# Kernel tuning notes

Measured on AMD Instinct MI355X. Metric: run time of the kernel, lower is better.

The kernel has to match this reference:

```python
import jax, jax.numpy as jnp
import numpy as np


def setup_inputs() -> dict:
    key = jax.random.key(0)
    ks = jax.random.split(key, 7)
    O, I, K = 64, 64, 3
    D = K * K
    x = jax.random.normal(ks[0], (32, I, 224, 224), jnp.float32)
    weight_loc = jax.random.normal(ks[1], (O, I, K, K), jnp.float32) * 0.05
    weight_L = jax.random.normal(ks[2], (O, I, D, D), jnp.float32) * 0.05
    bias_loc = jax.random.normal(ks[3], (O,), jnp.float32) * 0.05
    bias_ro = jax.random.normal(ks[4], (O,), jnp.float32) * 0.05
    eps_w = jax.random.normal(ks[5], (O, I, D), jnp.float32)
    eps_b = jax.random.normal(ks[6], (O,), jnp.float32)
    return {"x": x, "weight_loc": weight_loc, "weight_L": weight_L,
            "bias_loc": bias_loc, "bias_ro": bias_ro,
            "eps_w": eps_w, "eps_b": eps_b}


def reference(x, weight_loc, weight_L, bias_loc, bias_ro, eps_w, eps_b):
    # weight_loc: [O, I, K, K]; weight_L: [O, I, D, D] with D = K*K
    O, I, K, _ = weight_loc.shape
    D = K * K
    # diag_softplus: softplus on the diagonal of each per-(o,i) scale_tril,
    # keep strictly-lower part; MVN uses the lower-triangular scale_tril.
    diag = jnp.diagonal(weight_L, axis1=-2, axis2=-1)            # [O, I, D]
    eye = jnp.eye(D, dtype=weight_L.dtype)
    L = jnp.tril(weight_L, -1) + jax.nn.softplus(diag)[..., None] * eye  # [O, I, D, D]
    # Batched MVN rsample: loc + L @ eps, collapsing the O*I Python loop
    w = weight_loc + jnp.einsum('oiab,oib->oia', L, eps_w).reshape(O, I, K, K)
    # Bias rsample: loc + eps * softplus(ro)
    b = bias_loc + eps_b * jax.nn.softplus(bias_ro)              # [O]
    out = jax.lax.conv_general_dilated(
        x, w, window_strides=(1, 1), padding='SAME',
        dimension_numbers=('NCHW', 'OIHW', 'NCHW'))
    return out + b[None, :, None, None]
```

## Files before the change

### kernel.cpp

```cpp
#include <hip/hip_runtime.h>
#include <hip/hip_bf16.h>
#include <stdint.h>

typedef short bhalf8 __attribute__((ext_vector_type(8)));
typedef float facc4 __attribute__((ext_vector_type(4)));
typedef unsigned int uintv2 __attribute__((ext_vector_type(2)));

static __device__ __forceinline__ unsigned short f2bfu(float f) {
  return __builtin_bit_cast(unsigned short, __float2bfloat16(f));
}

__global__ void prep_kernel(const float* __restrict__ wloc,
                            const float* __restrict__ wL,
                            const float* __restrict__ eps_w,
                            const float* __restrict__ bloc,
                            const float* __restrict__ bro,
                            const float* __restrict__ eps_b,
                            short* __restrict__ wt, float* __restrict__ bias) {
  int t = blockIdx.x * 256 + threadIdx.x;
  int o = t >> 6, i = t & 63;
  int kc = i >> 5, il = i & 31;
  const float* Lp = wL + (size_t)t * 81;
  const float* ep = eps_w + (size_t)t * 9;
  const float* lp = wloc + (size_t)t * 9;
  float e[9];
#pragma unroll
  for (int b = 0; b < 9; ++b) e[b] = ep[b];
#pragma unroll
  for (int a = 0; a < 9; ++a) {
    float s = lp[a];
    for (int b = 0; b < a; ++b) s += Lp[a * 9 + b] * e[b];
    float d = Lp[a * 9 + a];
    float sp = (d > 20.f) ? d : log1pf(expf(d));
    s += sp * e[a];
    wt[((a * 2 + kc) * 64 + o) * 32 + il] = (short)f2bfu(s);
  }
  if (t < 64) {
    float d = bro[t];
    float sp = (d > 20.f) ? d : log1pf(expf(d));
    bias[t] = bloc[t] + eps_b[t] * sp;
  }
}

#define XBUF 10880

#define LD1(cj, i)                                                    \
  ((hok && (w_in0 + (i)) >= 0 && (w_in0 + (i)) < 224)                 \
       ? cbase[(size_t)(cj)*50176 + w_in0 + (i)]                      \
       : 0.f)

__global__ __launch_bounds__(512, 4) void conv_fused_kernel(
    const float* __restrict__ x, const short* __restrict__ wtg,
    const float* __restrict__ bias, float* __restrict__ out) {
  extern __shared__ short smem[];
  short* lds_x = smem;
  short* lds_w = smem + 21760;

  int b0 = blockIdx.x;
  int b = (b0 & 7) * 784 + (b0 >> 3);
  int ht = b % 28;
  int rest = b / 28;
  int wc = rest % 7, n = rest / 7;
  int h0 = ht * 8, w0 = wc * 32;
  int t = threadIdx.x, lane = t & 63, wv = t >> 6;
  int l15 = lane & 15, l4 = lane >> 4;

#define LOADX(V, ic_)                                                       \
  do {                                                                      \
    _Pragma("unroll") for (int k = 0; k < 2; ++k) {                         \
      int u = t + k * 512;                                                  \
      if (u < 720) {                                                        \
        int chg = u & 7, tmp = u >> 3;                                      \
        int ccg = tmp % 9, r = tmp / 9;                                     \
        int h_in = h0 - 1 + r;                                              \
        bool hok = (h_in >= 0) & (h_in < 224);                              \
        int w_in0 = w0 - 1 + ccg * 4;                                       \
        const float* cbase =                                                \
            x + ((size_t)(n * 64 + (ic_)*32 + chg * 4) * 224 +              \
                 (hok ? h_in : 0)) *                                        \
                    224;                                                    \
        if (hok && w_in0 >= 0 && w_in0 + 3 < 224) {                         \
          V[k][0] = *(const float4*)(cbase + w_in0);                        \
          V[k][1] = *(const float4*)(cbase + 50176 + w_in0);                \
          V[k][2] = *(const float4*)(cbase + 2 * 50176 + w_in0);            \
          V[k][3] = *(const float4*)(cbase + 3 * 50176 + w_in0);            \
        } else {                                                            \
          V[k][0] = make_float4(LD1(0, 0), LD1(0, 1), LD1(0, 2), LD1(0, 3)); \
          V[k][1] = make_float4(LD1(1, 0), LD1(1, 1), LD1(1, 2), LD1(1, 3)); \
          V[k][2] = make_float4(LD1(2, 0), LD1(2, 1), LD1(2, 2), LD1(2, 3)); \
          V[k][3] = make_float4(LD1(3, 0), LD1(3, 1), LD1(3, 2), LD1(3, 3)); \
        }                                                                   \
      }                                                                     \
    }                                                                       \
  } while (0)

#define CVTW(bufsel, V)                                                     \
  do {                                                                      \
    short* lx_ = lds_x + (bufsel)*XBUF;                                     \
    _Pragma("unroll") for (int k = 0; k < 2; ++k) {                         \
      int u = t + k * 512;                                                  \
      if (u < 720) {                                                        \
        int chg = u & 7, tmp = u >> 3;                                      \
        int ccg = tmp % 9, r = tmp / 9;                                     \
        int g = chg >> 1, hs = (chg & 1) << 2;                              \
        _Pragma("unroll") for (int i = 0; i < 4; ++i) {                     \
          int cc = ccg * 4 + i;                                             \
          if (cc < 34) {                                                    \
            float a0 = ((const float*)&V[k][0])[i];                         \
            float a1 = ((const float*)&V[k][1])[i];                         \
            float a2 = ((const float*)&V[k][2])[i];                         \
            float a3 = ((const float*)&V[k][3])[i];                         \
            unsigned int p0 =                                               \
                (unsigned int)f2bfu(a0) | ((unsigned int)f2bfu(a1) << 16);  \
            unsigned int p1 =                                               \
                (unsigned int)f2bfu(a2) | ((unsigned int)f2bfu(a3) << 16);  \
            uintv2 pk = {p0, p1};                                           \
            *(uintv2*)(lx_ + (((r * 4 + g) * 34 + cc) << 3) + hs) = pk;     \
          }                                                                 \
        }                                                                   \
      }                                                                     \
    }                                                                       \
  } while (0)

#define STAGE_W(ic_)                                                        \
  do {                                                                      \
    _Pragma("unroll") for (int k = 0; k < 5; ++k) {                         \
      int id = k * 512 + t;                                                 \
      if (id < 2304) {                                                      \
        int a_ = id >> 8, rem_ = id & 255;                                  \
        int g_ = rem_ >> 6, o_ = rem_ & 63;                                 \
        const short* src =                                                  \
            wtg + ((a_ * 2 + (ic_)) * 64 + o_) * 32 + g_ * 8;               \
        __builtin_amdgcn_global_load_lds(                                   \
            (const __attribute__((address_space(1))) void*)src,             \
            (__attribute__((address_space(3))) void*)(lds_w +               \
                                                      (k * 512 + wv * 64) * \
                                                          8),               \
            16, 0, 0);                                                      \
      }                                                                     \
    }                                                                       \
  } while (0)

  facc4 acc[4][2];
#pragma unroll
  for (int om = 0; om < 4; ++om)
#pragma unroll
    for (int p = 0; p < 2; ++p) {
      facc4 z = {0.f, 0.f, 0.f, 0.f};
      acc[om][p] = z;
    }

#define COMPUTE(bufsel)                                                     \
  do {                                                                      \
    const short* bx = lds_x + (bufsel)*XBUF;                                \
    __builtin_amdgcn_s_setprio(1);                                          \
    _Pragma("unroll") for (int kh = 0; kh < 3; ++kh) {                      \
      int r = wv + kh;                                                      \
      _Pragma("unroll") for (int kw = 0; kw < 3; ++kw) {                    \
        const int a_ = kh * 3 + kw;                                         \
        bhalf8 av[4];                                                       \
        _Pragma("unroll") for (int om = 0; om < 4; ++om) av[om] =           \
            *(const bhalf8*)(lds_w +                                        \
                             ((a_ * 4 + l4) * 64 + om * 16 + l15) * 8);     \
        _Pragma("unroll") for (int p = 0; p < 2; ++p) {                     \
          int tc = p * 16 + l15 + kw;                                       \
          bhalf8 bv = *(const bhalf8*)(bx + ((r * 4 + l4) * 34 + tc) * 8);  \
          _Pragma("unroll") for (int om = 0; om < 4; ++om) acc[om][p] =     \
              __builtin_amdgcn_mfma_f32_16x16x32_bf16(av[om], bv,           \
                                                      acc[om][p], 0, 0, 0); \
        }                                                                   \
      }                                                                     \
    }                                                                       \
    __builtin_amdgcn_s_setprio(0);                                          \
  } while (0)

  float4 xv[2][4];

  STAGE_W(0);
  LOADX(xv, 0);
  CVTW(0, xv);
  asm volatile("s_waitcnt vmcnt(0)" ::: "memory");
  __syncthreads();

  LOADX(xv, 1);
  __builtin_amdgcn_sched_barrier(0);
  COMPUTE(0);
  __builtin_amdgcn_s_barrier();
  __builtin_amdgcn_sched_barrier(0);
  STAGE_W(1);
  CVTW(1, xv);
  asm volatile("s_waitcnt vmcnt(0)" ::: "memory");
  __syncthreads();
  COMPUTE(1);

#undef LOADX
#undef CVTW
#undef STAGE_W
#undef COMPUTE

  int h = h0 + wv;
#pragma unroll
  for (int om = 0; om < 4; ++om) {
#pragma unroll
    for (int jj = 0; jj < 4; ++jj) {
      int o = om * 16 + l4 * 4 + jj;
      float bo = bias[o];
      float* op = out + ((size_t)(n * 64 + o) * 224 + h) * 224 + w0;
#pragma unroll
      for (int p = 0; p < 2; ++p) op[p * 16 + l15] = acc[om][p][jj] + bo;
    }
  }
}

extern "C" void kernel_launch(void* const* d_in, const int* in_sizes, int n_in,
                              void* d_out, int out_size, void* d_ws,
                              size_t ws_size, hipStream_t stream) {
  const float* x = (const float*)d_in[0];
  const float* wloc = (const float*)d_in[1];
  const float* wL = (const float*)d_in[2];
  const float* bloc = (const float*)d_in[3];
  const float* bro = (const float*)d_in[4];
  const float* eps_w = (const float*)d_in[5];
  const float* eps_b = (const float*)d_in[6];
  float* outp = (float*)d_out;

  short* wt = (short*)d_ws;
  float* bias = (float*)((char*)d_ws + 73728);

  prep_kernel<<<16, 256, 0, stream>>>(wloc, wL, eps_w, bloc, bro, eps_b, wt,
                                      bias);
  const int dyn_lds = (21760 + 18432) * 2;
  hipFuncSetAttribute((const void*)conv_fused_kernel,
                      hipFuncAttributeMaxDynamicSharedMemorySize, dyn_lds);
  conv_fused_kernel<<<6272, 512, dyn_lds, stream>>>(x, wt, bias, outp);
}
```

Measured before the change: 279.1 us.

## Make conv blocks persistent, sweeping width tiles with a double-buffered pipeline

Each block now handles a 7-row strip and loops over all 7 width tiles and both input-channel halves in a 14-step pipeline. It prefetches the next input tile into registers while computing from LDS, and writes results after every second step. The grid shrinks from 6272 blocks of 512 threads to 1024 blocks of 448 threads (7 waves), so launch and prologue costs are paid fewer times. The trade-off is that weights are re-staged every other step and fewer blocks may leave CUs underused or expose the pipeline's serial tail.

```diff
diff --git a/kernel.cpp b/kernel.cpp
--- a/kernel.cpp
+++ b/kernel.cpp
@@ -42,39 +42,37 @@
   }
 }
 
-#define XBUF 10880
+#define XBUF 9792
 
 #define LD1(cj, i)                                                    \
   ((hok && (w_in0 + (i)) >= 0 && (w_in0 + (i)) < 224)                 \
        ? cbase[(size_t)(cj)*50176 + w_in0 + (i)]                      \
        : 0.f)
 
-__global__ __launch_bounds__(512, 4) void conv_fused_kernel(
+__global__ __launch_bounds__(448, 4) void conv_sweep_kernel(
     const float* __restrict__ x, const short* __restrict__ wtg,
     const float* __restrict__ bias, float* __restrict__ out) {
   extern __shared__ short smem[];
   short* lds_x = smem;
-  short* lds_w = smem + 21760;
+  short* lds_w = smem + 19584;
 
   int b0 = blockIdx.x;
-  int b = (b0 & 7) * 784 + (b0 >> 3);
-  int ht = b % 28;
-  int rest = b / 28;
-  int wc = rest % 7, n = rest / 7;
-  int h0 = ht * 8, w0 = wc * 32;
+  int b = (b0 & 7) * 128 + (b0 >> 3);
+  int ht = b & 31, n = b >> 5;
+  int h0 = ht * 7;
   int t = threadIdx.x, lane = t & 63, wv = t >> 6;
   int l15 = lane & 15, l4 = lane >> 4;
 
-#define LOADX(V, ic_)                                                       \
+#define LOADX(V, wc_, ic_)                                                  \
   do {                                                                      \
     _Pragma("unroll") for (int k = 0; k < 2; ++k) {                         \
-      int u = t + k * 512;                                                  \
-      if (u < 720) {                                                        \
+      int u = t + k * 448;                                                  \
+      if (u < 648) {                                                        \
         int chg = u & 7, tmp = u >> 3;                                      \
         int ccg = tmp % 9, r = tmp / 9;                                     \
         int h_in = h0 - 1 + r;                                              \
         bool hok = (h_in >= 0) & (h_in < 224);                              \
-        int w_in0 = w0 - 1 + ccg * 4;                                       \
+        int w_in0 = (wc_)*32 - 1 + ccg * 4;                                 \
         const float* cbase =                                                \
             x + ((size_t)(n * 64 + (ic_)*32 + chg * 4) * 224 +              \
                  (hok ? h_in : 0)) *                                        \
@@ -98,8 +96,8 @@
   do {                                                                      \
     short* lx_ = lds_x + (bufsel)*XBUF;                                     \
     _Pragma("unroll") for (int k = 0; k < 2; ++k) {                         \
-      int u = t + k * 512;                                                  \
-      if (u < 720) {                                                        \
+      int u = t + k * 448;                                                  \
+      if (u < 648) {                                                        \
         int chg = u & 7, tmp = u >> 3;                                      \
         int ccg = tmp % 9, r = tmp / 9;                                     \
         int g = chg >> 1, hs = (chg & 1) << 2;                              \
@@ -124,8 +122,8 @@
 
 #define STAGE_W(ic_)                                                        \
   do {                                                                      \
-    _Pragma("unroll") for (int k = 0; k < 5; ++k) {                         \
-      int id = k * 512 + t;                                                 \
+    _Pragma("unroll") for (int k = 0; k < 6; ++k) {                         \
+      int id = k * 448 + t;                                                 \
       if (id < 2304) {                                                      \
         int a_ = id >> 8, rem_ = id & 255;                                  \
         int g_ = rem_ >> 6, o_ = rem_ & 63;                                 \
@@ -133,10 +131,8 @@
             wtg + ((a_ * 2 + (ic_)) * 64 + o_) * 32 + g_ * 8;               \
         __builtin_amdgcn_global_load_lds(                                   \
             (const __attribute__((address_space(1))) void*)src,             \
-            (__attribute__((address_space(3))) void*)(lds_w +               \
-                                                      (k * 512 + wv * 64) * \
-                                                          8),               \
-            16, 0, 0);                                                      \
+            (__attribute__((address_space(3))) void*)(lds_w + id * 8), 16,  \
+            0, 0);                                                          \
       }                                                                     \
     }                                                                       \
   } while (0)
@@ -177,39 +173,61 @@
   float4 xv[2][4];
 
   STAGE_W(0);
-  LOADX(xv, 0);
+  LOADX(xv, 0, 0);
   CVTW(0, xv);
   asm volatile("s_waitcnt vmcnt(0)" ::: "memory");
-  __syncthreads();
-
-  LOADX(xv, 1);
+  asm volatile("s_waitcnt lgkmcnt(0)" ::: "memory");
   __builtin_amdgcn_sched_barrier(0);
-  COMPUTE(0);
   __builtin_amdgcn_s_barrier();
   __builtin_amdgcn_sched_barrier(0);
-  STAGE_W(1);
-  CVTW(1, xv);
-  asm volatile("s_waitcnt vmcnt(0)" ::: "memory");
-  __syncthreads();
-  COMPUTE(1);
-
+
+#pragma unroll 1
+  for (int rr = 0; rr < 14; ++rr) {
+    const int icn = ((rr + 1) ^ ((rr + 1) >> 1)) & 1;
+    if (rr < 13) LOADX(xv, (rr + 1) >> 1, icn);
+    __builtin_amdgcn_sched_barrier(0);
+    COMPUTE(rr & 1);
+
+    if (rr & 1) {
+      const int w0_ = (rr >> 1) * 32;
+      int h = h0 + wv;
+#pragma unroll
+      for (int om = 0; om < 4; ++om) {
+#pragma unroll
+        for (int jj = 0; jj < 4; ++jj) {
+          int o = om * 16 + l4 * 4 + jj;
+          float bo = bias[o];
+          float* op = out + ((size_t)(n * 64 + o) * 224 + h) * 224 + w0_;
+#pragma unroll
+          for (int p = 0; p < 2; ++p) op[p * 16 + l15] = acc[om][p][jj] + bo;
+        }
+      }
+#pragma unroll
+      for (int om = 0; om < 4; ++om)
+#pragma unroll
+        for (int p = 0; p < 2; ++p) {
+          facc4 z = {0.f, 0.f, 0.f, 0.f};
+          acc[om][p] = z;
+        }
+    }
+
+    __builtin_amdgcn_s_barrier();
+    __builtin_amdgcn_sched_barrier(0);
+    if (rr < 13) {
+      CVTW((rr + 1) & 1, xv);
+      if (!(rr & 1)) STAGE_W(icn);
+      if (!(rr & 1))
+        asm volatile("s_waitcnt vmcnt(0)" ::: "memory");
+      asm volatile("s_waitcnt lgkmcnt(0)" ::: "memory");
+      __builtin_amdgcn_sched_barrier(0);
+      __builtin_amdgcn_s_barrier();
+      __builtin_amdgcn_sched_barrier(0);
+    }
+  }
 #undef LOADX
 #undef CVTW
 #undef STAGE_W
 #undef COMPUTE
-
-  int h = h0 + wv;
-#pragma unroll
-  for (int om = 0; om < 4; ++om) {
-#pragma unroll
-    for (int jj = 0; jj < 4; ++jj) {
-      int o = om * 16 + l4 * 4 + jj;
-      float bo = bias[o];
-      float* op = out + ((size_t)(n * 64 + o) * 224 + h) * 224 + w0;
-#pragma unroll
-      for (int p = 0; p < 2; ++p) op[p * 16 + l15] = acc[om][p][jj] + bo;
-    }
-  }
 }
 
 extern "C" void kernel_launch(void* const* d_in, const int* in_sizes, int n_in,
@@ -229,8 +247,8 @@
 
   prep_kernel<<<16, 256, 0, stream>>>(wloc, wL, eps_w, bloc, bro, eps_b, wt,
                                       bias);
-  const int dyn_lds = (21760 + 18432) * 2;
-  hipFuncSetAttribute((const void*)conv_fused_kernel,
+  const int dyn_lds = (2 * XBUF + 18432) * 2;
+  hipFuncSetAttribute((const void*)conv_sweep_kernel,
                       hipFuncAttributeMaxDynamicSharedMemorySize, dyn_lds);
-  conv_fused_kernel<<<6272, 512, dyn_lds, stream>>>(x, wt, bias, outp);
-}
+  conv_sweep_kernel<<<1024, 448, dyn_lds, stream>>>(x, wt, bias, outp);
+}
```

Result: slower. 431.0 us (+54.4%).
